# Kernel optimization log

Hardware: AMD Instinct MI355X
Metric: run time of the kernel (lower is better)

The kernel has to match this reference:

```python
import jax, jax.numpy as jnp
import numpy as np

EPS_DIST = 1e-8
EPS_BN = 1e-5


def _bn_relu(x, g, b):
    # training-mode BatchNorm1d over (batch, spatial) per channel, then ReLU
    mean = jnp.mean(x, axis=(0, 2), keepdims=True)
    var = jnp.mean((x - mean) ** 2, axis=(0, 2), keepdims=True)
    xhat = (x - mean) * jax.lax.rsqrt(var + EPS_BN)
    return jax.nn.relu(xhat * g[None, :, None] + b[None, :, None])


def setup_inputs() -> dict:
    key = jax.random.key(0)
    ks = jax.random.split(key, 8)
    B, N, M, C1, C2 = 8, 16384, 4096, 64, 256
    return {
        "p1": jax.random.normal(ks[0], (B, N, 3), jnp.float32),
        "p2": jax.random.normal(ks[1], (B, M, 3), jnp.float32),
        "f1": jax.random.normal(ks[2], (B, C1, N), jnp.float32),
        "f2": jax.random.normal(ks[3], (B, C2, M), jnp.float32),
        "idx": jax.random.randint(ks[4], (B, N, 3), 0, M, jnp.int64),
        "W1": jax.random.normal(ks[5], (256, C1 + C2), jnp.float32) * 0.05,
        "g1": jnp.ones((256,), jnp.float32),
        "b1": jnp.zeros((256,), jnp.float32),
        "W2": jax.random.normal(ks[6], (256, 256), jnp.float32) * 0.05,
        "g2": jnp.ones((256,), jnp.float32),
        "b2": jnp.zeros((256,), jnp.float32),
    }


def reference(p1, p2, f1, f2, idx, W1, g1, b1, W2, g2, b2):
    B = p1.shape[0]
    b_ix = jnp.arange(B)[:, None, None]  # batch index for gathers
    # --- three_interpolation: inverse-squared-distance weighted 3-NN interp ---
    nbr_xyz = p2[b_ix, idx]                     # [B, N, 3, 3]
    d2 = jnp.sum((p1[:, :, None, :] - nbr_xyz) ** 2, axis=-1)  # [B, N, 3]
    recip = 1.0 / (d2 + EPS_DIST)
    weight = recip / jnp.sum(recip, axis=-1, keepdims=True)    # [B, N, 3]
    f2_nbr = jnp.swapaxes(f2, 1, 2)[b_ix, idx]  # [B, N, 3, C2]
    interp = jnp.einsum("bnkc,bnk->bcn", f2_nbr, weight)       # [B, C2, N]
    # --- concat + two 1x1 conv + BN + ReLU blocks ---
    x = jnp.concatenate((f1, interp), axis=1)   # [B, C1+C2, N]
    x = _bn_relu(jnp.einsum("oi,bin->bon", W1, x), g1, b1)
    x = _bn_relu(jnp.einsum("oi,bin->bon", W2, x), g2, b2)
    return x
```

## Files before the change

kernel.cpp:

```cpp
#include <hip/hip_runtime.h>
#include <hip/hip_bf16.h>

#define BB 8
#define NN 16384
#define MM 4096
#define C1 64
#define C2 256
#define K1 320
#define CO 256
#define MTOT (BB * NN)

#define STATS_OFF 0
#define FLAG_OFF  8192
#define W1B_OFF   16384
#define W2B_OFF   180224
#define F2T_OFF   327680
#define XT_OFF    (327680 + 16777216)
#define H2_OFF    (327680 + 16777216 + 83886080)

typedef short v8s __attribute__((ext_vector_type(8)));
typedef float v4f __attribute__((ext_vector_type(4)));

__device__ __forceinline__ float bf2f(unsigned short u) {
    unsigned v = ((unsigned)u) << 16;
    float f;
    __builtin_memcpy(&f, &v, 4);
    return f;
}
__device__ __forceinline__ unsigned short f2bf(float f) {
    unsigned u;
    __builtin_memcpy(&u, &f, 4);
    unsigned r = u + 0x7fffu + ((u >> 16) & 1u);
    return (unsigned short)(r >> 16);
}
__device__ __forceinline__ void gload16(const unsigned short* g, unsigned short* l) {
    __builtin_amdgcn_global_load_lds((const __attribute__((address_space(1))) unsigned int*)g,
                                     (__attribute__((address_space(3))) unsigned int*)l, 16, 0, 0);
}

__global__ void k_prep(const void* idx_raw, int* flag64, float* stats,
                       const float* __restrict__ W1, unsigned short* __restrict__ W1b,
                       const float* __restrict__ W2, unsigned short* __restrict__ W2b) {
    int blk = blockIdx.x;
    int t = threadIdx.x;
    if (blk < 320) {
        int e = blk * 256 + t;
        W1b[e] = f2bf(W1[e]);
    } else if (blk < 576) {
        int e = (blk - 320) * 256 + t;
        W2b[e] = f2bf(W2[e]);
    } else {
        for (int i = t; i < 8 * 256; i += 256) stats[i] = 0.f;
        if (t == 0) {
            const int* a = (const int*)idx_raw;
            int all0 = 1;
            for (int j = 1; j < 64; j += 2) all0 &= (a[j] == 0);
            *flag64 = all0;
        }
    }
}

__global__ void k_tr_f2(const float* __restrict__ f2, unsigned short* __restrict__ f2t) {
    __shared__ float tile[32][33];
    int b = blockIdx.z;
    int c0 = blockIdx.y * 32;
    int m0 = blockIdx.x * 32;
    int tx = threadIdx.x, ty = threadIdx.y;
    const float* src = f2 + ((size_t)b * C2 + c0) * MM + m0;
#pragma unroll
    for (int j = 0; j < 4; ++j)
        tile[ty + 8 * j][tx] = src[(size_t)(ty + 8 * j) * MM + tx];
    __syncthreads();
    unsigned short* dst = f2t + ((size_t)b * MM + m0) * C2 + c0;
#pragma unroll
    for (int j = 0; j < 4; ++j)
        dst[(size_t)(ty + 8 * j) * C2 + tx] = f2bf(tile[tx][ty + 8 * j]);
}

__global__ void k_tr_f1(const float* __restrict__ f1, unsigned short* __restrict__ xT) {
    __shared__ float tile[32][33];
    int b = blockIdx.z;
    int c0 = blockIdx.y * 32;
    int n0 = blockIdx.x * 32;
    int tx = threadIdx.x, ty = threadIdx.y;
    const float* src = f1 + ((size_t)b * C1 + c0) * NN + n0;
#pragma unroll
    for (int j = 0; j < 4; ++j)
        tile[ty + 8 * j][tx] = src[(size_t)(ty + 8 * j) * NN + tx];
    __syncthreads();
    unsigned short* dst = xT + ((size_t)b * NN + n0) * K1 + c0;
#pragma unroll
    for (int j = 0; j < 4; ++j)
        dst[(size_t)(ty + 8 * j) * K1 + tx] = f2bf(tile[tx][ty + 8 * j]);
}

__global__ void k_interp(const float* __restrict__ p1, const float* __restrict__ p2,
                         const void* __restrict__ idxv, const int* __restrict__ flag64,
                         const unsigned short* __restrict__ f2t,
                         unsigned short* __restrict__ xT) {
    int t = threadIdx.x;
    int p = t >> 5, lane = t & 31;
    size_t pt = (size_t)blockIdx.x * 8 + p;
    int b = (int)(pt >> 14);
    int m0, m1, m2;
    if (*flag64) {
        const long long* id = (const long long*)idxv;
        m0 = (int)id[pt * 3 + 0]; m1 = (int)id[pt * 3 + 1]; m2 = (int)id[pt * 3 + 2];
    } else {
        const int* id = (const int*)idxv;
        m0 = id[pt * 3 + 0]; m1 = id[pt * 3 + 1]; m2 = id[pt * 3 + 2];
    }
    float qx = p1[pt * 3 + 0], qy = p1[pt * 3 + 1], qz = p1[pt * 3 + 2];
    const float* pb = p2 + (size_t)b * MM * 3;
    float dx, dy, dz;
    dx = qx - pb[m0 * 3 + 0]; dy = qy - pb[m0 * 3 + 1]; dz = qz - pb[m0 * 3 + 2];
    float d0 = dx * dx + dy * dy + dz * dz;
    dx = qx - pb[m1 * 3 + 0]; dy = qy - pb[m1 * 3 + 1]; dz = qz - pb[m1 * 3 + 2];
    float d1 = dx * dx + dy * dy + dz * dz;
    dx = qx - pb[m2 * 3 + 0]; dy = qy - pb[m2 * 3 + 1]; dz = qz - pb[m2 * 3 + 2];
    float d2v = dx * dx + dy * dy + dz * dz;
    float r0 = 1.f / (d0 + 1e-8f), r1 = 1.f / (d1 + 1e-8f), r2 = 1.f / (d2v + 1e-8f);
    float inv = 1.f / (r0 + r1 + r2);
    float w0 = r0 * inv, w1 = r1 * inv, w2 = r2 * inv;

    const unsigned short* fb = f2t + (size_t)b * MM * C2;
    int c0 = lane * 8;
    uint4 va = *(const uint4*)(fb + (size_t)m0 * C2 + c0);
    uint4 vb = *(const uint4*)(fb + (size_t)m1 * C2 + c0);
    uint4 vc = *(const uint4*)(fb + (size_t)m2 * C2 + c0);

    float r[8];
    {
        const unsigned av[4] = {va.x, va.y, va.z, va.w};
        const unsigned bv[4] = {vb.x, vb.y, vb.z, vb.w};
        const unsigned cv[4] = {vc.x, vc.y, vc.z, vc.w};
#pragma unroll
        for (int q = 0; q < 4; ++q) {
            r[2 * q + 0] = w0 * bf2f((unsigned short)(av[q] & 0xffff))
                         + w1 * bf2f((unsigned short)(bv[q] & 0xffff))
                         + w2 * bf2f((unsigned short)(cv[q] & 0xffff));
            r[2 * q + 1] = w0 * bf2f((unsigned short)(av[q] >> 16))
                         + w1 * bf2f((unsigned short)(bv[q] >> 16))
                         + w2 * bf2f((unsigned short)(cv[q] >> 16));
        }
    }
    uint4 outv;
    outv.x = (unsigned)f2bf(r[0]) | ((unsigned)f2bf(r[1]) << 16);
    outv.y = (unsigned)f2bf(r[2]) | ((unsigned)f2bf(r[3]) << 16);
    outv.z = (unsigned)f2bf(r[4]) | ((unsigned)f2bf(r[5]) << 16);
    outv.w = (unsigned)f2bf(r[6]) | ((unsigned)f2bf(r[7]) << 16);
    *(uint4*)(xT + pt * K1 + C1 + c0) = outv;
}

#define TM 128
#define TN 128
#define TK 64
__launch_bounds__(256)
__global__ void k_gemm1(const unsigned short* __restrict__ xT,
                        const unsigned short* __restrict__ W1b,
                        unsigned short* __restrict__ h1,
                        float* __restrict__ sum1, float* __restrict__ ssq1) {
    __shared__ unsigned short As[TM * TK];
    __shared__ unsigned short Bs[TN * TK];
    __shared__ float s_sum[TN], s_ssq[TN];
    const int t = threadIdx.x;
    const int lane = t & 63, w = t >> 6;
    const int wm = w >> 1, wc = w & 1;
    const long rbase = (long)blockIdx.x * TM;
    const int cb = blockIdx.y * TN;

    if (t < TN) { s_sum[t] = 0.f; s_ssq[t] = 0.f; }

    v4f acc[4][4];
#pragma unroll
    for (int r = 0; r < 4; ++r)
#pragma unroll
        for (int c = 0; c < 4; ++c) acc[r][c] = (v4f)(0.f);

    const int srow = w * 32 + (lane >> 3);
    const int sch = (lane & 7) * 8;
    const unsigned short* Ag = xT + (rbase + srow) * K1 + sch;
    const unsigned short* Bg = W1b + (size_t)(cb + srow) * K1 + sch;

    for (int k0 = 0; k0 < K1; k0 += TK) {
#pragma unroll
        for (int j = 0; j < 4; ++j) {
            gload16(Ag + (size_t)(j * 8) * K1 + k0, As + (w * 32 + j * 8) * TK);
            gload16(Bg + (size_t)(j * 8) * K1 + k0, Bs + (w * 32 + j * 8) * TK);
        }
        __syncthreads();
        const unsigned short* ApL = As + (wm * 64 + (lane & 15)) * TK + (lane >> 4) * 8;
        const unsigned short* BpL = Bs + (wc * 64 + (lane & 15)) * TK + (lane >> 4) * 8;
#pragma unroll
        for (int ks = 0; ks < 2; ++ks) {
            v8s af[4], bg[4];
#pragma unroll
            for (int r = 0; r < 4; ++r) af[r] = *(const v8s*)(ApL + r * 16 * TK + ks * 32);
#pragma unroll
            for (int c = 0; c < 4; ++c) bg[c] = *(const v8s*)(BpL + c * 16 * TK + ks * 32);
#pragma unroll
            for (int r = 0; r < 4; ++r)
#pragma unroll
                for (int c = 0; c < 4; ++c)
                    acc[r][c] = __builtin_amdgcn_mfma_f32_16x16x32_bf16(af[r], bg[c], acc[r][c], 0, 0, 0);
        }
        __syncthreads();
    }

    const int q = lane >> 4, ln = lane & 15;
#pragma unroll
    for (int c = 0; c < 4; ++c) {
        int col = cb + wc * 64 + c * 16 + ln;
        float s = 0.f, sq = 0.f;
#pragma unroll
        for (int r = 0; r < 4; ++r) {
            long row = rbase + wm * 64 + r * 16 + q * 4;
#pragma unroll
            for (int i = 0; i < 4; ++i) {
                float v = acc[r][c][i];
                h1[(size_t)(row + i) * CO + col] = f2bf(v);
                s += v; sq += v * v;
            }
        }
        atomicAdd(&s_sum[wc * 64 + c * 16 + ln], s);
        atomicAdd(&s_ssq[wc * 64 + c * 16 + ln], sq);
    }
    __syncthreads();
    if (t < TN) {
        atomicAdd(&sum1[cb + t], s_sum[t]);
        atomicAdd(&ssq1[cb + t], s_ssq[t]);
    }
}

__global__ void k_bnfin(const float* __restrict__ sum, const float* __restrict__ ssq,
                        const float* __restrict__ g, const float* __restrict__ bb,
                        float* __restrict__ scale, float* __restrict__ shift) {
    int c = threadIdx.x;
    const float invn = 1.f / (float)MTOT;
    float m = sum[c] * invn;
    float v = ssq[c] * invn - m * m;
    float s = g[c] * rsqrtf(v + 1e-5f);
    scale[c] = s;
    shift[c] = bb[c] - m * s;
}

__launch_bounds__(256)
__global__ void k_gemm2(const unsigned short* __restrict__ h1,
                        const unsigned short* __restrict__ W2b,
                        const float* __restrict__ scale1, const float* __restrict__ shift1,
                        unsigned short* __restrict__ h2,
                        float* __restrict__ sum2, float* __restrict__ ssq2) {
    __shared__ unsigned short As[TM * TK];
    __shared__ unsigned short Bs[TN * TK];
    __shared__ float s_sum[TN], s_ssq[TN];
    const int t = threadIdx.x;
    const int lane = t & 63, w = t >> 6;
    const int wm = w >> 1, wc = w & 1;
    const long rbase = (long)blockIdx.x * TM;
    const int cb = blockIdx.y * TN;

    if (t < TN) { s_sum[t] = 0.f; s_ssq[t] = 0.f; }

    v4f acc[4][4];
#pragma unroll
    for (int r = 0; r < 4; ++r)
#pragma unroll
        for (int c = 0; c < 4; ++c) acc[r][c] = (v4f)(0.f);

    const int srow = w * 32 + (lane >> 3);
    const int sch = (lane & 7) * 8;
    const unsigned short* Ag = h1 + (rbase + srow) * CO + sch;
    const unsigned short* Bg = W2b + (size_t)(cb + srow) * CO + sch;
    unsigned short* AsW = As + (srow)*TK + sch;

    for (int k0 = 0; k0 < CO; k0 += TK) {
#pragma unroll
        for (int j = 0; j < 4; ++j)
            gload16(Bg + (size_t)(j * 8) * CO + k0, Bs + (w * 32 + j * 8) * TK);
        float4 sca = *(const float4*)(scale1 + k0 + sch);
        float4 scb = *(const float4*)(scale1 + k0 + sch + 4);
        float4 sha = *(const float4*)(shift1 + k0 + sch);
        float4 shb = *(const float4*)(shift1 + k0 + sch + 4);
#pragma unroll
        for (int j = 0; j < 4; ++j) {
            uint4 av = *(const uint4*)(Ag + (size_t)(j * 8) * CO + k0);
            float y0 = fmaxf(bf2f((unsigned short)(av.x & 0xffff)) * sca.x + sha.x, 0.f);
            float y1 = fmaxf(bf2f((unsigned short)(av.x >> 16)) * sca.y + sha.y, 0.f);
            float y2 = fmaxf(bf2f((unsigned short)(av.y & 0xffff)) * sca.z + sha.z, 0.f);
            float y3 = fmaxf(bf2f((unsigned short)(av.y >> 16)) * sca.w + sha.w, 0.f);
            float y4 = fmaxf(bf2f((unsigned short)(av.z & 0xffff)) * scb.x + shb.x, 0.f);
            float y5 = fmaxf(bf2f((unsigned short)(av.z >> 16)) * scb.y + shb.y, 0.f);
            float y6 = fmaxf(bf2f((unsigned short)(av.w & 0xffff)) * scb.z + shb.z, 0.f);
            float y7 = fmaxf(bf2f((unsigned short)(av.w >> 16)) * scb.w + shb.w, 0.f);
            uint4 ov;
            ov.x = (unsigned)f2bf(y0) | ((unsigned)f2bf(y1) << 16);
            ov.y = (unsigned)f2bf(y2) | ((unsigned)f2bf(y3) << 16);
            ov.z = (unsigned)f2bf(y4) | ((unsigned)f2bf(y5) << 16);
            ov.w = (unsigned)f2bf(y6) | ((unsigned)f2bf(y7) << 16);
            *(uint4*)(AsW + (j * 8) * TK) = ov;
        }
        __syncthreads();
        const unsigned short* ApL = As + (wm * 64 + (lane & 15)) * TK + (lane >> 4) * 8;
        const unsigned short* BpL = Bs + (wc * 64 + (lane & 15)) * TK + (lane >> 4) * 8;
#pragma unroll
        for (int ks = 0; ks < 2; ++ks) {
            v8s af[4], bg4[4];
#pragma unroll
            for (int r = 0; r < 4; ++r) af[r] = *(const v8s*)(ApL + r * 16 * TK + ks * 32);
#pragma unroll
            for (int c = 0; c < 4; ++c) bg4[c] = *(const v8s*)(BpL + c * 16 * TK + ks * 32);
#pragma unroll
            for (int r = 0; r < 4; ++r)
#pragma unroll
                for (int c = 0; c < 4; ++c)
                    acc[r][c] = __builtin_amdgcn_mfma_f32_16x16x32_bf16(af[r], bg4[c], acc[r][c], 0, 0, 0);
        }
        __syncthreads();
    }

    const int q = lane >> 4, ln = lane & 15;
    const int b = (int)(rbase >> 14);
    const int nb = (int)(rbase & (NN - 1)) + wm * 64;
#pragma unroll
    for (int c = 0; c < 4; ++c) {
        int o = cb + wc * 64 + c * 16 + ln;
        unsigned short* hp = h2 + (((size_t)(b * CO + o)) << 14);
        float s = 0.f, sq = 0.f;
#pragma unroll
        for (int r = 0; r < 4; ++r) {
            int n0 = nb + r * 16 + q * 4;
            float v0 = acc[r][c][0], v1 = acc[r][c][1], v2 = acc[r][c][2], v3 = acc[r][c][3];
            ushort4 hv;
            hv.x = f2bf(v0); hv.y = f2bf(v1); hv.z = f2bf(v2); hv.w = f2bf(v3);
            *(ushort4*)(hp + n0) = hv;
            s += v0 + v1 + v2 + v3;
            sq += v0 * v0 + v1 * v1 + v2 * v2 + v3 * v3;
        }
        atomicAdd(&s_sum[wc * 64 + c * 16 + ln], s);
        atomicAdd(&s_ssq[wc * 64 + c * 16 + ln], sq);
    }
    __syncthreads();
    if (t < TN) {
        atomicAdd(&sum2[cb + t], s_sum[t]);
        atomicAdd(&ssq2[cb + t], s_ssq[t]);
    }
}

__global__ void k_apply(const unsigned short* __restrict__ h2,
                        const float* __restrict__ scale2, const float* __restrict__ shift2,
                        float* __restrict__ out) {
    size_t i = ((size_t)blockIdx.x * 256 + threadIdx.x) * 4;
    int o = (int)((i >> 14) & 255);
    float s = scale2[o], d = shift2[o];
    ushort4 hv = *(const ushort4*)(h2 + i);
    float4 v;
    v.x = fmaxf(bf2f(hv.x) * s + d, 0.f);
    v.y = fmaxf(bf2f(hv.y) * s + d, 0.f);
    v.z = fmaxf(bf2f(hv.z) * s + d, 0.f);
    v.w = fmaxf(bf2f(hv.w) * s + d, 0.f);
    *(float4*)&out[i] = v;
}

extern "C" void kernel_launch(void* const* d_in, const int* in_sizes, int n_in,
                              void* d_out, int out_size, void* d_ws, size_t ws_size,
                              hipStream_t stream) {
    const float* p1 = (const float*)d_in[0];
    const float* p2 = (const float*)d_in[1];
    const float* f1 = (const float*)d_in[2];
    const float* f2 = (const float*)d_in[3];
    const void*  idx = d_in[4];
    const float* W1 = (const float*)d_in[5];
    const float* g1 = (const float*)d_in[6];
    const float* b1 = (const float*)d_in[7];
    const float* W2 = (const float*)d_in[8];
    const float* g2 = (const float*)d_in[9];
    const float* b2 = (const float*)d_in[10];
    float* out = (float*)d_out;

    char* ws = (char*)d_ws;
    float* stats = (float*)(ws + STATS_OFF);
    float* sum1 = stats + 0;     float* ssq1 = stats + 256;
    float* scale1 = stats + 512; float* shift1 = stats + 768;
    float* sum2 = stats + 1024;  float* ssq2 = stats + 1280;
    float* scale2 = stats + 1536; float* shift2 = stats + 1792;
    int* flag64 = (int*)(ws + FLAG_OFF);
    unsigned short* W1b = (unsigned short*)(ws + W1B_OFF);
    unsigned short* W2b = (unsigned short*)(ws + W2B_OFF);
    unsigned short* f2t = (unsigned short*)(ws + F2T_OFF);
    unsigned short* xT  = (unsigned short*)(ws + XT_OFF);
    unsigned short* h2  = (unsigned short*)(ws + H2_OFF);

    unsigned short* h1 = (unsigned short*)d_out;

    k_prep<<<577, 256, 0, stream>>>(idx, flag64, stats, W1, W1b, W2, W2b);
    k_tr_f2<<<dim3(MM / 32, C2 / 32, BB), dim3(32, 8), 0, stream>>>(f2, f2t);
    k_tr_f1<<<dim3(NN / 32, C1 / 32, BB), dim3(32, 8), 0, stream>>>(f1, xT);
    k_interp<<<MTOT / 8, 256, 0, stream>>>(p1, p2, idx, flag64, f2t, xT);
    k_gemm1<<<dim3(MTOT / TM, CO / TN), 256, 0, stream>>>(xT, W1b, h1, sum1, ssq1);
    k_bnfin<<<1, 256, 0, stream>>>(sum1, ssq1, g1, b1, scale1, shift1);
    k_gemm2<<<dim3(MTOT / TM, CO / TN), 256, 0, stream>>>(h1, W2b, scale1, shift1, h2, sum2, ssq2);
    k_bnfin<<<1, 256, 0, stream>>>(sum2, ssq2, g2, b2, scale2, shift2);
    k_apply<<<(int)((size_t)out_size / 4 / 256), 256, 0, stream>>>(h2, scale2, shift2, out);
}
```

Measured before the change: 433.0 us.

## Stage GEMM epilogues through swizzled LDS, widen transposes, fold BN finalize into consumers

The GEMM1 and GEMM2 epilogues now write bf16 results into swizzled shared memory and then emit coalesced 16-byte row stores, replacing scattered 2-byte and 8-byte global writes. The f1 and f2 transpose kernels use 64-channel tiles with vectorized uint4 bf16 stores. The two single-block BN-finalize launches are removed: each GEMM2 block and each apply block recomputes scale and shift from the raw sums. This cuts launches and uncoalesced stores, at the cost of redundant per-block finalize work and an extra LDS round trip plus barrier in each epilogue.

```diff
diff --git a/kernel.cpp b/kernel.cpp
--- a/kernel.cpp
+++ b/kernel.cpp
@@ -61,37 +61,50 @@
 }
 
 __global__ void k_tr_f2(const float* __restrict__ f2, unsigned short* __restrict__ f2t) {
-    __shared__ float tile[32][33];
+    __shared__ float tile[64][33];
     int b = blockIdx.z;
-    int c0 = blockIdx.y * 32;
+    int c0 = blockIdx.y * 64;
     int m0 = blockIdx.x * 32;
-    int tx = threadIdx.x, ty = threadIdx.y;
+    int t = threadIdx.x;
+    int lm = t & 31, lc = t >> 5;
     const float* src = f2 + ((size_t)b * C2 + c0) * MM + m0;
 #pragma unroll
-    for (int j = 0; j < 4; ++j)
-        tile[ty + 8 * j][tx] = src[(size_t)(ty + 8 * j) * MM + tx];
-    __syncthreads();
-    unsigned short* dst = f2t + ((size_t)b * MM + m0) * C2 + c0;
-#pragma unroll
-    for (int j = 0; j < 4; ++j)
-        dst[(size_t)(ty + 8 * j) * C2 + tx] = f2bf(tile[tx][ty + 8 * j]);
+    for (int j = 0; j < 8; ++j)
+        tile[lc + 8 * j][lm] = src[(size_t)(lc + 8 * j) * MM + lm];
+    __syncthreads();
+    int m = t >> 3, c8 = (t & 7) * 8;
+    unsigned short tmp[8];
+#pragma unroll
+    for (int k = 0; k < 8; ++k) tmp[k] = f2bf(tile[c8 + k][m]);
+    uint4 v;
+    v.x = (unsigned)tmp[0] | ((unsigned)tmp[1] << 16);
+    v.y = (unsigned)tmp[2] | ((unsigned)tmp[3] << 16);
+    v.z = (unsigned)tmp[4] | ((unsigned)tmp[5] << 16);
+    v.w = (unsigned)tmp[6] | ((unsigned)tmp[7] << 16);
+    *(uint4*)&f2t[((size_t)b * MM + m0 + m) * C2 + c0 + c8] = v;
 }
 
 __global__ void k_tr_f1(const float* __restrict__ f1, unsigned short* __restrict__ xT) {
-    __shared__ float tile[32][33];
+    __shared__ float tile[64][33];
     int b = blockIdx.z;
-    int c0 = blockIdx.y * 32;
     int n0 = blockIdx.x * 32;
-    int tx = threadIdx.x, ty = threadIdx.y;
-    const float* src = f1 + ((size_t)b * C1 + c0) * NN + n0;
-#pragma unroll
-    for (int j = 0; j < 4; ++j)
-        tile[ty + 8 * j][tx] = src[(size_t)(ty + 8 * j) * NN + tx];
-    __syncthreads();
-    unsigned short* dst = xT + ((size_t)b * NN + n0) * K1 + c0;
-#pragma unroll
-    for (int j = 0; j < 4; ++j)
-        dst[(size_t)(ty + 8 * j) * K1 + tx] = f2bf(tile[tx][ty + 8 * j]);
+    int t = threadIdx.x;
+    int lm = t & 31, lc = t >> 5;
+    const float* src = f1 + ((size_t)b * C1) * NN + n0;
+#pragma unroll
+    for (int j = 0; j < 8; ++j)
+        tile[lc + 8 * j][lm] = src[(size_t)(lc + 8 * j) * NN + lm];
+    __syncthreads();
+    int m = t >> 3, c8 = (t & 7) * 8;
+    unsigned short tmp[8];
+#pragma unroll
+    for (int k = 0; k < 8; ++k) tmp[k] = f2bf(tile[c8 + k][m]);
+    uint4 v;
+    v.x = (unsigned)tmp[0] | ((unsigned)tmp[1] << 16);
+    v.y = (unsigned)tmp[2] | ((unsigned)tmp[3] << 16);
+    v.z = (unsigned)tmp[4] | ((unsigned)tmp[5] << 16);
+    v.w = (unsigned)tmp[6] | ((unsigned)tmp[7] << 16);
+    *(uint4*)&xT[((size_t)b * NN + n0 + m) * K1 + c8] = v;
 }
 
 __global__ void k_interp(const float* __restrict__ p1, const float* __restrict__ p2,
@@ -160,9 +173,10 @@
                         const unsigned short* __restrict__ W1b,
                         unsigned short* __restrict__ h1,
                         float* __restrict__ sum1, float* __restrict__ ssq1) {
-    __shared__ unsigned short As[TM * TK];
-    __shared__ unsigned short Bs[TN * TK];
+    __shared__ unsigned short smem[TM * TK + TN * TK];
     __shared__ float s_sum[TN], s_ssq[TN];
+    unsigned short* As = smem;
+    unsigned short* Bs = smem + TM * TK;
     const int t = threadIdx.x;
     const int lane = t & 63, w = t >> 6;
     const int wm = w >> 1, wc = w & 1;
@@ -210,56 +224,65 @@
     const int q = lane >> 4, ln = lane & 15;
 #pragma unroll
     for (int c = 0; c < 4; ++c) {
-        int col = cb + wc * 64 + c * 16 + ln;
+        int col = wc * 64 + c * 16 + ln;
+        int cc = col >> 3, ci = col & 7;
         float s = 0.f, sq = 0.f;
 #pragma unroll
-        for (int r = 0; r < 4; ++r) {
-            long row = rbase + wm * 64 + r * 16 + q * 4;
+        for (int r = 0; r < 4; ++r)
 #pragma unroll
             for (int i = 0; i < 4; ++i) {
+                int row = wm * 64 + r * 16 + q * 4 + i;
                 float v = acc[r][c][i];
-                h1[(size_t)(row + i) * CO + col] = f2bf(v);
+                smem[row * 128 + 8 * (cc ^ (row & 15)) + ci] = f2bf(v);
                 s += v; sq += v * v;
             }
-        }
-        atomicAdd(&s_sum[wc * 64 + c * 16 + ln], s);
-        atomicAdd(&s_ssq[wc * 64 + c * 16 + ln], sq);
-    }
-    __syncthreads();
+        atomicAdd(&s_sum[col], s);
+        atomicAdd(&s_ssq[col], sq);
+    }
+    __syncthreads();
+    {
+        int rr = t >> 4, cc2 = t & 15;
+#pragma unroll
+        for (int j = 0; j < 8; ++j) {
+            int row = rr + 16 * j;
+            uint4 v = *(const uint4*)&smem[row * 128 + 8 * (cc2 ^ (row & 15))];
+            *(uint4*)&h1[(size_t)(rbase + row) * CO + cb + cc2 * 8] = v;
+        }
+    }
     if (t < TN) {
         atomicAdd(&sum1[cb + t], s_sum[t]);
         atomicAdd(&ssq1[cb + t], s_ssq[t]);
     }
 }
 
-__global__ void k_bnfin(const float* __restrict__ sum, const float* __restrict__ ssq,
-                        const float* __restrict__ g, const float* __restrict__ bb,
-                        float* __restrict__ scale, float* __restrict__ shift) {
-    int c = threadIdx.x;
-    const float invn = 1.f / (float)MTOT;
-    float m = sum[c] * invn;
-    float v = ssq[c] * invn - m * m;
-    float s = g[c] * rsqrtf(v + 1e-5f);
-    scale[c] = s;
-    shift[c] = bb[c] - m * s;
-}
-
 __launch_bounds__(256)
 __global__ void k_gemm2(const unsigned short* __restrict__ h1,
                         const unsigned short* __restrict__ W2b,
-                        const float* __restrict__ scale1, const float* __restrict__ shift1,
+                        const float* __restrict__ sum1, const float* __restrict__ ssq1,
+                        const float* __restrict__ g1, const float* __restrict__ b1,
                         unsigned short* __restrict__ h2,
                         float* __restrict__ sum2, float* __restrict__ ssq2) {
-    __shared__ unsigned short As[TM * TK];
-    __shared__ unsigned short Bs[TN * TK];
+    __shared__ unsigned short smem[TM * TK + TN * TK];
     __shared__ float s_sum[TN], s_ssq[TN];
+    __shared__ float sc1[CO], sh1[CO];
+    unsigned short* As = smem;
+    unsigned short* Bs = smem + TM * TK;
     const int t = threadIdx.x;
     const int lane = t & 63, w = t >> 6;
     const int wm = w >> 1, wc = w & 1;
     const long rbase = (long)blockIdx.x * TM;
     const int cb = blockIdx.y * TN;
 
+    {
+        const float invn = 1.f / (float)MTOT;
+        float m = sum1[t] * invn;
+        float v = ssq1[t] * invn - m * m;
+        float s = g1[t] * rsqrtf(v + 1e-5f);
+        sc1[t] = s;
+        sh1[t] = b1[t] - m * s;
+    }
     if (t < TN) { s_sum[t] = 0.f; s_ssq[t] = 0.f; }
+    __syncthreads();
 
     v4f acc[4][4];
 #pragma unroll
@@ -271,16 +294,16 @@
     const int sch = (lane & 7) * 8;
     const unsigned short* Ag = h1 + (rbase + srow) * CO + sch;
     const unsigned short* Bg = W2b + (size_t)(cb + srow) * CO + sch;
-    unsigned short* AsW = As + (srow)*TK + sch;
+    unsigned short* AsW = As + srow * TK + sch;
 
     for (int k0 = 0; k0 < CO; k0 += TK) {
 #pragma unroll
         for (int j = 0; j < 4; ++j)
             gload16(Bg + (size_t)(j * 8) * CO + k0, Bs + (w * 32 + j * 8) * TK);
-        float4 sca = *(const float4*)(scale1 + k0 + sch);
-        float4 scb = *(const float4*)(scale1 + k0 + sch + 4);
-        float4 sha = *(const float4*)(shift1 + k0 + sch);
-        float4 shb = *(const float4*)(shift1 + k0 + sch + 4);
+        float4 sca = *(const float4*)(sc1 + k0 + sch);
+        float4 scb = *(const float4*)(sc1 + k0 + sch + 4);
+        float4 sha = *(const float4*)(sh1 + k0 + sch);
+        float4 shb = *(const float4*)(sh1 + k0 + sch + 4);
 #pragma unroll
         for (int j = 0; j < 4; ++j) {
             uint4 av = *(const uint4*)(Ag + (size_t)(j * 8) * CO + k0);
@@ -320,26 +343,34 @@
 
     const int q = lane >> 4, ln = lane & 15;
     const int b = (int)(rbase >> 14);
-    const int nb = (int)(rbase & (NN - 1)) + wm * 64;
+    const int nb = (int)(rbase & (NN - 1));
 #pragma unroll
     for (int c = 0; c < 4; ++c) {
-        int o = cb + wc * 64 + c * 16 + ln;
-        unsigned short* hp = h2 + (((size_t)(b * CO + o)) << 14);
+        int ol = wc * 64 + c * 16 + ln;
         float s = 0.f, sq = 0.f;
 #pragma unroll
-        for (int r = 0; r < 4; ++r) {
-            int n0 = nb + r * 16 + q * 4;
-            float v0 = acc[r][c][0], v1 = acc[r][c][1], v2 = acc[r][c][2], v3 = acc[r][c][3];
-            ushort4 hv;
-            hv.x = f2bf(v0); hv.y = f2bf(v1); hv.z = f2bf(v2); hv.w = f2bf(v3);
-            *(ushort4*)(hp + n0) = hv;
-            s += v0 + v1 + v2 + v3;
-            sq += v0 * v0 + v1 * v1 + v2 * v2 + v3 * v3;
-        }
-        atomicAdd(&s_sum[wc * 64 + c * 16 + ln], s);
-        atomicAdd(&s_ssq[wc * 64 + c * 16 + ln], sq);
-    }
-    __syncthreads();
+        for (int r = 0; r < 4; ++r)
+#pragma unroll
+            for (int i = 0; i < 4; ++i) {
+                int row = wm * 64 + r * 16 + q * 4 + i;
+                int rc = row >> 3, ri = row & 7;
+                float v = acc[r][c][i];
+                smem[ol * 128 + 8 * (rc ^ (ol & 15)) + ri] = f2bf(v);
+                s += v; sq += v * v;
+            }
+        atomicAdd(&s_sum[ol], s);
+        atomicAdd(&s_ssq[ol], sq);
+    }
+    __syncthreads();
+    {
+        int oo = t >> 4, nc = t & 15;
+#pragma unroll
+        for (int j = 0; j < 8; ++j) {
+            int ol = oo + 16 * j;
+            uint4 v = *(const uint4*)&smem[ol * 128 + 8 * (nc ^ (ol & 15))];
+            *(uint4*)&h2[(((size_t)(b * CO + cb + ol)) << 14) + nb + nc * 8] = v;
+        }
+    }
     if (t < TN) {
         atomicAdd(&sum2[cb + t], s_sum[t]);
         atomicAdd(&ssq2[cb + t], s_ssq[t]);
@@ -347,11 +378,22 @@
 }
 
 __global__ void k_apply(const unsigned short* __restrict__ h2,
-                        const float* __restrict__ scale2, const float* __restrict__ shift2,
+                        const float* __restrict__ sum2, const float* __restrict__ ssq2,
+                        const float* __restrict__ g2, const float* __restrict__ b2,
                         float* __restrict__ out) {
+    __shared__ float ss[2];
+    int o = (blockIdx.x >> 4) & 255;
+    if (threadIdx.x == 0) {
+        const float invn = 1.f / (float)MTOT;
+        float m = sum2[o] * invn;
+        float v = ssq2[o] * invn - m * m;
+        float s = g2[o] * rsqrtf(v + 1e-5f);
+        ss[0] = s;
+        ss[1] = b2[o] - m * s;
+    }
+    __syncthreads();
+    float s = ss[0], d = ss[1];
     size_t i = ((size_t)blockIdx.x * 256 + threadIdx.x) * 4;
-    int o = (int)((i >> 14) & 255);
-    float s = scale2[o], d = shift2[o];
     ushort4 hv = *(const ushort4*)(h2 + i);
     float4 v;
     v.x = fmaxf(bf2f(hv.x) * s + d, 0.f);
@@ -380,9 +422,7 @@
     char* ws = (char*)d_ws;
     float* stats = (float*)(ws + STATS_OFF);
     float* sum1 = stats + 0;     float* ssq1 = stats + 256;
-    float* scale1 = stats + 512; float* shift1 = stats + 768;
     float* sum2 = stats + 1024;  float* ssq2 = stats + 1280;
-    float* scale2 = stats + 1536; float* shift2 = stats + 1792;
     int* flag64 = (int*)(ws + FLAG_OFF);
     unsigned short* W1b = (unsigned short*)(ws + W1B_OFF);
     unsigned short* W2b = (unsigned short*)(ws + W2B_OFF);
@@ -393,12 +433,10 @@
     unsigned short* h1 = (unsigned short*)d_out;
 
     k_prep<<<577, 256, 0, stream>>>(idx, flag64, stats, W1, W1b, W2, W2b);
-    k_tr_f2<<<dim3(MM / 32, C2 / 32, BB), dim3(32, 8), 0, stream>>>(f2, f2t);
-    k_tr_f1<<<dim3(NN / 32, C1 / 32, BB), dim3(32, 8), 0, stream>>>(f1, xT);
+    k_tr_f2<<<dim3(MM / 32, C2 / 64, BB), 256, 0, stream>>>(f2, f2t);
+    k_tr_f1<<<dim3(NN / 32, 1, BB), 256, 0, stream>>>(f1, xT);
     k_interp<<<MTOT / 8, 256, 0, stream>>>(p1, p2, idx, flag64, f2t, xT);
     k_gemm1<<<dim3(MTOT / TM, CO / TN), 256, 0, stream>>>(xT, W1b, h1, sum1, ssq1);
-    k_bnfin<<<1, 256, 0, stream>>>(sum1, ssq1, g1, b1, scale1, shift1);
-    k_gemm2<<<dim3(MTOT / TM, CO / TN), 256, 0, stream>>>(h1, W2b, scale1, shift1, h2, sum2, ssq2);
-    k_bnfin<<<1, 256, 0, stream>>>(sum2, ssq2, g2, b2, scale2, shift2);
-    k_apply<<<(int)((size_t)out_size / 4 / 256), 256, 0, stream>>>(h2, scale2, shift2, out);
-}
+    k_gemm2<<<dim3(MTOT / TM, CO / TN), 256, 0, stream>>>(h1, W2b, sum1, ssq1, g1, b1, h2, sum2, ssq2);
+    k_apply<<<(int)((size_t)out_size / 4 / 256), 256, 0, stream>>>(h2, sum2, ssq2, g2, b2, out);
+}
```

New measurement: 425.9 us. No clear change (-1.6%).
